# Optimization experiments

Measured on AMD Instinct MI355X. Metric: run time of the kernel, lower is better.

Reference implementation:

```python
import jax, jax.numpy as jnp
import numpy as np

B, N, DIM, HEADS, DH = 2, 1024, 1024, 16, 64
SEQ_LEN, MEM_NUM = 1024, 4
EH, EW, ET = 4, 4, 1  # mem_expand_size
PH, PW = 4, 4        # patch grid
CUR_PATCH_IDX = 5
MEM_IDXS = [0, 1, 4, 5]


def _locate(idx):
    # get_pos_from_idx_down_right
    num_frame = PH * PW
    inner = idx % num_frame
    return (inner % PH, inner // PH, idx // num_frame)


def _rel_idxs():
    rph, rpw = 2 * EH + 1, 2 * EW + 1
    frame = rph * rpw
    src = _locate(CUR_PATCH_IDX)
    out = []
    for t in MEM_IDXS + [CUR_PATCH_IDX]:
        tg = _locate(t)
        out.append((tg[0] - src[0] + EH) * rpw + (tg[1] - src[1] + EW) + (tg[2] - src[2] + ET) * frame)
    return np.array(out, np.int32)


def setup_inputs() -> dict:
    key = jax.random.key(0)
    ks = jax.random.split(key, 8)
    inner = HEADS * DH
    s = 0.02
    return {
        "x": jax.random.normal(ks[0], (B, N, DIM), jnp.float32),
        "mem": jax.random.normal(ks[1], (B, MEM_NUM * SEQ_LEN, DIM), jnp.float32),
        "mask": jnp.zeros((B, MEM_NUM * SEQ_LEN + N), bool),
        "rel_idxs": jnp.asarray(_rel_idxs()),
        "Wq": jax.random.normal(ks[2], (DIM, inner), jnp.float32) * s,
        "Wk": jax.random.normal(ks[3], (DIM, inner), jnp.float32) * s,
        "Wv": jax.random.normal(ks[4], (DIM, inner), jnp.float32) * s,
        "Wo": jax.random.normal(ks[5], (inner, DIM), jnp.float32) * s,
        "bo": jnp.zeros((DIM,), jnp.float32),
        "rel_table": jax.random.normal(ks[6], ((2 * EH + 1) * (2 * EW + 1) * (2 * ET + 1), HEADS), jnp.float32) * s,
    }


def reference(x, mem, mask, rel_idxs, Wq, Wk, Wv, Wo, bo, rel_table):
    b, n, dim = x.shape
    heads = rel_table.shape[1]
    dh = Wq.shape[1] // heads
    mem_num = rel_idxs.shape[0] - 1
    mem_len = mem.shape[1]
    seq_len = mem_len // mem_num
    scale = dh ** (-0.5)

    kx = jnp.concatenate([mem, x], axis=1)           # [b, j, dim]
    j = kx.shape[1]
    q = (x @ Wq).reshape(b, n, heads, dh).transpose(0, 2, 1, 3)   # bhid
    k = (kx @ Wk).reshape(b, j, heads, dh).transpose(0, 2, 1, 3)  # bhjd
    v = (kx @ Wv).reshape(b, j, heads, dh).transpose(0, 2, 1, 3)

    # relative position bias: a per-head scalar added to every K feature
    rel_emb = rel_table[rel_idxs].T                  # [h, mem_num+1]
    bias_mem = jnp.repeat(rel_emb[:, :mem_num], seq_len, axis=1)  # [h, mem_len]
    bias_cur = jnp.broadcast_to(rel_emb[:, -1:], (heads, j - mem_len))
    bias = jnp.concatenate([bias_mem, bias_cur], axis=1)          # [h, j]
    k = k + bias[None, :, :, None]

    dots = jnp.einsum('bhid,bhjd->bhij', q, k) * scale
    neg = -jnp.finfo(dots.dtype).max
    dots = jnp.where(mask[:, None, None, :], neg, dots)
    causal = jnp.triu(jnp.ones((n, j), bool), j - n + 1)
    dots = jnp.where(causal, neg, dots)

    attn = jax.nn.softmax(dots, axis=-1)
    out = jnp.einsum('bhij,bhjd->bhid', attn, v)
    out = out.transpose(0, 2, 1, 3).reshape(b, n, heads * dh) @ Wo + bo
    new_mem = x[:, -seq_len:]
    return out, new_mem
```

## Files before the change

kernel.cpp:

```cpp
#include <hip/hip_runtime.h>
#include <float.h>

#define NQ    1024
#define JTOT  5120
#define MEML  4096
#define SCL2  0.18033688011112042f

typedef __attribute__((ext_vector_type(8))) short bf16x8;
typedef __attribute__((ext_vector_type(8))) unsigned short ush8;
typedef __attribute__((ext_vector_type(4))) unsigned short ush4;
typedef __attribute__((ext_vector_type(4))) float f32x4;

static __device__ __forceinline__ unsigned short f2bf(float x) {
    union { float f; unsigned u; } v; v.f = x;
    unsigned r = (v.u + 0x7fffu + ((v.u >> 16) & 1u)) >> 16;
    return (unsigned short)r;
}
static __device__ __forceinline__ unsigned pack2(float f0, float f1) {
    union { float f; unsigned u; } a, b; a.f = f1; b.f = f0;
    return __builtin_amdgcn_perm(a.u, b.u, 0x07060302u);
}

static __device__ __forceinline__ void gld16(const void* g, void* l) {
    __builtin_amdgcn_global_load_lds(
        (const __attribute__((address_space(1))) unsigned int*)g,
        (__attribute__((address_space(3))) unsigned int*)l, 16, 0, 0);
}

__global__ __launch_bounds__(256)
void prep_kernel(const float* __restrict__ x, const float* __restrict__ mem,
                 const unsigned char* __restrict__ mask,
                 const float* __restrict__ W0, const float* __restrict__ W1,
                 const float* __restrict__ W2, const float* __restrict__ W3,
                 unsigned short* __restrict__ xb, unsigned short* __restrict__ memb,
                 unsigned short* __restrict__ wt, float* __restrict__ mbp)
{
    __shared__ float Ts[32][33];
    const int bid = blockIdx.x;
    const int t   = threadIdx.x;
    if (bid < 5120) {
        const float* src = (bid < 1024) ? x : mem;
        unsigned short* dst = (bid < 1024) ? xb : memb;
        const size_t i = (size_t)((bid < 1024) ? bid : bid - 1024) * 2048 + t * 8;
        float4 a = *(const float4*)(src + i);
        float4 b = *(const float4*)(src + i + 4);
        ush8 o;
        o[0] = f2bf(a.x); o[1] = f2bf(a.y); o[2] = f2bf(a.z); o[3] = f2bf(a.w);
        o[4] = f2bf(b.x); o[5] = f2bf(b.y); o[6] = f2bf(b.z); o[7] = f2bf(b.w);
        *(ush8*)(dst + i) = o;
    } else if (bid < 5160) {
        const int i = (bid - 5120) * 256 + t;
        mbp[i] = mask[i] ? -1.0e30f : 0.0f;
    } else {
        const int idx = bid - 5160;
        const int z   = idx >> 10;
        const int rem = idx & 1023;
        const float* W = (z == 0) ? W0 : (z == 1) ? W1 : (z == 2) ? W2 : W3;
        unsigned short* D = wt + (size_t)z * 1024 * 1024;
        const int n0 = (rem & 31) * 32, k0 = (rem >> 5) * 32;
        const int tr = t >> 3, tc = (t & 7) * 4;
        float4 v = *(const float4*)(W + (size_t)(k0 + tr) * 1024 + n0 + tc);
        Ts[tr][tc + 0] = v.x; Ts[tr][tc + 1] = v.y;
        Ts[tr][tc + 2] = v.z; Ts[tr][tc + 3] = v.w;
        __syncthreads();
        ush4 o;
        o[0] = f2bf(Ts[tc + 0][tr]); o[1] = f2bf(Ts[tc + 1][tr]);
        o[2] = f2bf(Ts[tc + 2][tr]); o[3] = f2bf(Ts[tc + 3][tr]);
        *(ush4*)(D + (size_t)(n0 + tr) * 1024 + k0 + tc) = o;
    }
}

__global__ __launch_bounds__(512, 2)
void mgemm01_kernel(const unsigned short* __restrict__ xb,
                    const unsigned short* __restrict__ memb,
                    const unsigned short* __restrict__ wt,
                    unsigned short* __restrict__ Qb, unsigned short* __restrict__ Kb,
                    unsigned short* __restrict__ Vb,
                    const float* __restrict__ rel_table, const int* __restrict__ rel_idxs)
{
    __shared__ unsigned short A1R0[128 * 64], A2R0[128 * 64];
    __shared__ unsigned short A1R1[128 * 64], A2R1[128 * 64];
    __shared__ unsigned short Bf0[256 * 64],  Bf1[256 * 64];

    const int t    = threadIdx.x;
    const int lane = t & 63;
    const int w    = t >> 6;
    const int wr   = w >> 2;
    const int wc   = w & 3;
    const int l15  = lane & 15;
    const int quad = lane >> 4;
    const int l7   = l15 & 7;
    const int srow = lane >> 3;
    const int scol = ((lane & 7) ^ srow) << 3;

    const int bid = blockIdx.x;
    int mode, bx, by;
    if (bid < 96) {
        mode = 0;
        const int l = (bid & 7) * 12 + (bid >> 3);
        bx = l >> 3;
        by = l & 7;
    } else {
        mode = 1;
        const int p   = bid - 96;
        const int xcd = p & 7;
        const int i   = p >> 3;
        bx = i & 7;
        by = (xcd << 2) + (i >> 3);
    }
    const int mat = bx >> 2;
    const int n0  = (bx & 3) << 8;
    const int m0  = by << 8;
    const unsigned short* Ag = (mode == 0) ? xb : memb;
    const unsigned short* Bg = wt + (size_t)((mode == 0) ? mat : mat + 1) * 1024 * 1024;

    const size_t abase = (size_t)(m0 + srow) * 1024 + scol;
    const size_t bbase = (size_t)(n0 + srow) * 1024 + scol;

    auto stgB0 = [&](unsigned short* BO, int kt) {
        const int kb = kt << 6, r0 = w * 16;
        gld16(Bg + bbase + (size_t)r0 * 1024 + kb,       BO + r0 * 64);
        gld16(Bg + bbase + (size_t)(r0 + 8) * 1024 + kb, BO + (r0 + 8) * 64);
    };
    auto stgB1 = [&](unsigned short* BO, int kt) {
        const int kb = kt << 6, r0 = 128 + w * 16;
        gld16(Bg + bbase + (size_t)r0 * 1024 + kb,       BO + r0 * 64);
        gld16(Bg + bbase + (size_t)(r0 + 8) * 1024 + kb, BO + (r0 + 8) * 64);
    };
    auto stgA1 = [&](unsigned short* AO, int kt) {
        const int kb = kt << 6, r0 = w * 8;
        gld16(Ag + abase + (size_t)r0 * 1024 + kb,         AO + r0 * 64);
        gld16(Ag + abase + (size_t)(128 + r0) * 1024 + kb, AO + (64 + r0) * 64);
    };
    auto stgA2 = [&](unsigned short* AO, int kt) {
        const int kb = kt << 6, r0 = w * 8;
        gld16(Ag + abase + (size_t)(64 + r0) * 1024 + kb,  AO + r0 * 64);
        gld16(Ag + abase + (size_t)(192 + r0) * 1024 + kb, AO + (64 + r0) * 64);
    };

    f32x4 acc[8][4];
    #pragma unroll
    for (int i = 0; i < 8; i++)
        #pragma unroll
        for (int j = 0; j < 4; j++) acc[i][j] = (f32x4){0.f, 0.f, 0.f, 0.f};

    stgB0(Bf0, 0); stgB1(Bf0, 0); stgA1(A1R0, 0); stgA2(A2R0, 0);
    stgB0(Bf1, 1); stgA1(A1R1, 1); stgB1(Bf1, 1);
    asm volatile("s_waitcnt vmcnt(6)");
    __builtin_amdgcn_s_barrier();

    bf16x8 bfr[4][2];

#define PHASE(AO, MB, STAGE, VMW)                                                  \
    {                                                                              \
        const int Ra0 = (wr * 64 + ((MB) & 3) * 16 + l15) * 64;                    \
        const int Ra1 = Ra0 + 16 * 64;                                             \
        const bf16x8 a0 = *(const bf16x8*)&AO[Ra0 + ((quad ^ l7) << 3)];           \
        const bf16x8 a1 = *(const bf16x8*)&AO[Ra0 + (((4 | quad) ^ l7) << 3)];     \
        const bf16x8 a2 = *(const bf16x8*)&AO[Ra1 + ((quad ^ l7) << 3)];           \
        const bf16x8 a3 = *(const bf16x8*)&AO[Ra1 + (((4 | quad) ^ l7) << 3)];     \
        STAGE;                                                                     \
        __builtin_amdgcn_s_barrier();                                              \
        asm volatile("s_waitcnt lgkmcnt(0)");                                      \
        __builtin_amdgcn_sched_barrier(0);                                         \
        __builtin_amdgcn_s_setprio(1);                                             \
        _Pragma("unroll")                                                          \
        for (int n = 0; n < 4; n++) {                                              \
            acc[(MB)][n]     = __builtin_amdgcn_mfma_f32_16x16x32_bf16(a0, bfr[n][0], acc[(MB)][n], 0, 0, 0);     \
            acc[(MB)][n]     = __builtin_amdgcn_mfma_f32_16x16x32_bf16(a1, bfr[n][1], acc[(MB)][n], 0, 0, 0);     \
            acc[(MB) + 1][n] = __builtin_amdgcn_mfma_f32_16x16x32_bf16(a2, bfr[n][0], acc[(MB) + 1][n], 0, 0, 0); \
            acc[(MB) + 1][n] = __builtin_amdgcn_mfma_f32_16x16x32_bf16(a3, bfr[n][1], acc[(MB) + 1][n], 0, 0, 0); \
        }                                                                          \
        __builtin_amdgcn_s_setprio(0);                                             \
        VMW;                                                                       \
        __builtin_amdgcn_s_barrier();                                              \
    }

#define KSTEP(A1O, A2O, BO, S0, S1, S2, S3, VMW)                                   \
    {                                                                              \
        _Pragma("unroll")                                                          \
        for (int n = 0; n < 4; n++) {                                              \
            const int Rb = (wc * 64 + n * 16 + l15) * 64;                          \
            bfr[n][0] = *(const bf16x8*)&BO[Rb + ((quad ^ l7) << 3)];              \
            bfr[n][1] = *(const bf16x8*)&BO[Rb + (((4 | quad) ^ l7) << 3)];        \
        }                                                                          \
        PHASE(A1O, 0, S0, (void)0)                                                 \
        PHASE(A1O, 2, S1, (void)0)                                                 \
        PHASE(A2O, 4, S2, (void)0)                                                 \
        PHASE(A2O, 6, S3, VMW)                                                     \
    }

    for (int e = 0; e < 14; e += 2) {
        KSTEP(A1R0, A2R0, Bf0,
              stgA2(A2R1, e + 1),
              stgB0(Bf0, e + 2),
              stgA1(A1R0, e + 2),
              stgB1(Bf0, e + 2),
              asm volatile("s_waitcnt vmcnt(6)"))
        KSTEP(A1R1, A2R1, Bf1,
              stgA2(A2R0, e + 2),
              stgB0(Bf1, e + 3),
              stgA1(A1R1, e + 3),
              stgB1(Bf1, e + 3),
              asm volatile("s_waitcnt vmcnt(6)"))
    }
    KSTEP(A1R0, A2R0, Bf0, stgA2(A2R1, 15), (void)0, (void)0, (void)0,
          asm volatile("s_waitcnt vmcnt(0)"))
    KSTEP(A1R1, A2R1, Bf1, (void)0, (void)0, (void)0, (void)0, (void)0)

#undef KSTEP
#undef PHASE

    const bool isQ = (mode == 0) && (mat == 0);
    const bool isK = (mode == 0) ? (mat == 1) : (mat == 0);
    if (!isQ && !isK) {
        #pragma unroll
        for (int m = 0; m < 8; m++) {
            const int r0 = m0 + wr * 128 + m * 16 + quad * 4;
            const int bb = (mode == 0) ? (r0 >> 10) : (r0 >> 12);
            const int j0 = (mode == 0) ? 4096 + (r0 & 1023) : (r0 & 4095);
            #pragma unroll
            for (int n = 0; n < 4; n++) {
                const int col = n0 + wc * 64 + n * 16 + l15;
                ush4 o;
                o[0] = f2bf(acc[m][n][0]); o[1] = f2bf(acc[m][n][1]);
                o[2] = f2bf(acc[m][n][2]); o[3] = f2bf(acc[m][n][3]);
                *(ush4*)(Vb + ((size_t)((bb * 16 + (col >> 6)) * 64 + (col & 63))) * JTOT + j0) = o;
            }
        }
    } else {
        #pragma unroll
        for (int m = 0; m < 8; m++)
            #pragma unroll
            for (int reg = 0; reg < 4; reg++) {
                const int r = m0 + wr * 128 + m * 16 + quad * 4 + reg;
                int bb, idx, chunk;
                if (mode == 0) { bb = r >> 10; idx = isK ? 4096 + (r & 1023) : (r & 1023); chunk = 4; }
                else           { bb = r >> 12; idx = r & 4095; chunk = idx >> 10; }
                #pragma unroll
                for (int n = 0; n < 4; n++) {
                    const int col = n0 + wc * 64 + n * 16 + l15;
                    const int hh = col >> 6, dh = col & 63;
                    float v = acc[m][n][reg];
                    if (isK) {
                        v += rel_table[rel_idxs[chunk] * 16 + hh];
                        Kb[((size_t)(bb * 16 + hh) * JTOT + idx) * 64 + dh] = f2bf(v);
                    } else {
                        Qb[((size_t)(bb * 16 + hh) * NQ + idx) * 64 + dh] = f2bf(v);
                    }
                }
            }
    }
}

__global__ __launch_bounds__(256)
void mgemm2_kernel(const unsigned short* __restrict__ A,
                   const unsigned short* __restrict__ WT,
                   float* __restrict__ outF, const float* __restrict__ bo,
                   const float* __restrict__ x, float* __restrict__ newmem)
{
    __shared__ unsigned short Al[64 * 64];
    __shared__ unsigned short Bl[128 * 64];

    const int t = threadIdx.x;
    if (blockIdx.z == 1) {
        const int blk = blockIdx.y * 8 + blockIdx.x;
        const size_t base = (size_t)blk * 8192 + t * 4;
        #pragma unroll
        for (int i = 0; i < 8; i++)
            *(float4*)(newmem + base + (size_t)i * 1024) =
                *(const float4*)(x + base + (size_t)i * 1024);
        return;
    }

    const int lane = t & 63;
    const int w    = t >> 6;
    const int l15  = lane & 15;
    const int quad = lane >> 4;
    const int l7   = l15 & 7;
    const int n0   = blockIdx.x * 128;
    const int m0   = blockIdx.y * 64;

    f32x4 acc[4][2];
    #pragma unroll
    for (int i = 0; i < 4; i++)
        #pragma unroll
        for (int j = 0; j < 2; j++) acc[i][j] = (f32x4){0.f, 0.f, 0.f, 0.f};

    for (int k0 = 0; k0 < 1024; k0 += 64) {
        __syncthreads();
        #pragma unroll
        for (int it = 0; it < 2; it++) {
            const int lin  = it * 256 + t;
            const int row  = lin >> 3;
            const int colb = ((lin & 7) ^ (row & 7)) * 8;
            gld16(A + (size_t)(m0 + row) * 1024 + k0 + colb,
                  &Al[(size_t)(it * 256 + w * 64) * 8]);
        }
        #pragma unroll
        for (int it = 0; it < 4; it++) {
            const int lin  = it * 256 + t;
            const int row  = lin >> 3;
            const int colb = ((lin & 7) ^ (row & 7)) * 8;
            gld16(WT + (size_t)(n0 + row) * 1024 + k0 + colb,
                  &Bl[(size_t)(it * 256 + w * 64) * 8]);
        }
        __syncthreads();
        bf16x8 af[4][2], bfr[2][2];
        #pragma unroll
        for (int i = 0; i < 4; i++) {
            const int R = i * 16 + l15;
            af[i][0] = *(const bf16x8*)&Al[R * 64 + ((quad ^ l7) << 3)];
            af[i][1] = *(const bf16x8*)&Al[R * 64 + (((4 | quad) ^ l7) << 3)];
        }
        #pragma unroll
        for (int j = 0; j < 2; j++) {
            const int R = w * 32 + j * 16 + l15;
            bfr[j][0] = *(const bf16x8*)&Bl[R * 64 + ((quad ^ l7) << 3)];
            bfr[j][1] = *(const bf16x8*)&Bl[R * 64 + (((4 | quad) ^ l7) << 3)];
        }
        #pragma unroll
        for (int i = 0; i < 4; i++)
            #pragma unroll
            for (int j = 0; j < 2; j++) {
                acc[i][j] = __builtin_amdgcn_mfma_f32_16x16x32_bf16(af[i][0], bfr[j][0], acc[i][j], 0, 0, 0);
                acc[i][j] = __builtin_amdgcn_mfma_f32_16x16x32_bf16(af[i][1], bfr[j][1], acc[i][j], 0, 0, 0);
            }
    }

    #pragma unroll
    for (int i = 0; i < 4; i++)
        #pragma unroll
        for (int reg = 0; reg < 4; reg++) {
            const int r = m0 + i * 16 + quad * 4 + reg;
            #pragma unroll
            for (int j = 0; j < 2; j++) {
                const int col = n0 + w * 32 + j * 16 + l15;
                outF[(size_t)r * 1024 + col] = acc[i][j][reg] + bo[col];
            }
        }
}

__global__ __launch_bounds__(256)
void attn5_kernel(const unsigned short* __restrict__ qh,
                  const unsigned short* __restrict__ kh,
                  const unsigned short* __restrict__ vt,
                  const float* __restrict__ mb,
                  unsigned short* __restrict__ ao)
{
    __shared__ unsigned short Ks[128 * 64];
    __shared__ unsigned short Vs[64 * 128];
    __shared__ unsigned short Ps[64 * 128];

    const int t    = threadIdx.x;
    const int lane = t & 63;
    const int w    = t >> 6;
    const int l15  = lane & 15;
    const int quad = lane >> 4;
    const int l7   = l15 & 7;
    const int qt   = blockIdx.x;
    const int h    = blockIdx.y;
    const int b    = blockIdx.z;
    const int qbase = qt * 64;
    const int qg    = qbase + w * 16 + l15;

    const unsigned short* qrow = qh + (((size_t)(b * 16 + h) * NQ + qg) << 6);
    const bf16x8 bq0 = *(const bf16x8*)(qrow + quad * 8);
    const bf16x8 bq1 = *(const bf16x8*)(qrow + 32 + quad * 8);

    const int krow = t >> 3;
    const int kcol = (t & 7) * 8;
    const int ksw  = ((t & 7) ^ (krow & 7)) * 8;
    const int vrow = t >> 4;
    const int vu   = t & 15;
    const int vcol = vu * 8;
    const int vsw  = ((vu & 8) | ((vu ^ (vrow & 7)) & 7)) * 8;

    const unsigned short* kbase = kh + (((size_t)(b * 16 + h) * JTOT) << 6);
    const unsigned short* vbase = vt + (((size_t)(b * 16 + h)) << 6) * JTOT;
    const float* mbb = mb + b * JTOT;

    f32x4 oa[4];
    #pragma unroll
    for (int mt = 0; mt < 4; mt++) oa[mt] = (f32x4){0.f, 0.f, 0.f, 0.f};
    float l_i = 0.f;

    const int ntp = (qt + 66) >> 1;

    ush8 kst[4], vst[4];
    #pragma unroll
    for (int p = 0; p < 4; p++)
        kst[p] = *(const ush8*)(kbase + ((size_t)(krow + 32 * p) << 6) + kcol);
    #pragma unroll
    for (int p = 0; p < 4; p++)
        vst[p] = *(const ush8*)(vbase + (size_t)(vrow + 16 * p) * JTOT + vcol);

    for (int jt = 0; jt < ntp; jt++) {
        const int jbase = jt * 128;
        __syncthreads();
        #pragma unroll
        for (int p = 0; p < 4; p++)
            *(ush8*)&Ks[(krow + 32 * p) * 64 + ksw] = kst[p];
        #pragma unroll
        for (int p = 0; p < 4; p++)
            *(ush8*)&Vs[(vrow + 16 * p) * 128 + vsw] = vst[p];
        __syncthreads();

        if (jt + 1 < ntp) {
            const int jb2 = jbase + 128;
            #pragma unroll
            for (int p = 0; p < 4; p++)
                kst[p] = *(const ush8*)(kbase + ((size_t)(jb2 + krow + 32 * p) << 6) + kcol);
            #pragma unroll
            for (int p = 0; p < 4; p++)
                vst[p] = *(const ush8*)(vbase + (size_t)(vrow + 16 * p) * JTOT + jb2 + vcol);
        }

        f32x4 sa[8];
        __builtin_amdgcn_s_setprio(1);
        #pragma unroll
        for (int mt2 = 0; mt2 < 8; mt2++) {
            const int ra = (mt2 * 16 + l15) * 64;
            const bf16x8 ak0 = *(const bf16x8*)&Ks[ra + ((quad ^ l7) << 3)];
            const bf16x8 ak1 = *(const bf16x8*)&Ks[ra + (((4 | quad) ^ l7) << 3)];
            f32x4 s = (f32x4){0.f, 0.f, 0.f, 0.f};
            s = __builtin_amdgcn_mfma_f32_16x16x32_bf16(ak0, bq0, s, 0, 0, 0);
            s = __builtin_amdgcn_mfma_f32_16x16x32_bf16(ak1, bq1, s, 0, 0, 0);
            sa[mt2] = s;
        }
        __builtin_amdgcn_s_setprio(0);

        #pragma unroll
        for (int mt2 = 0; mt2 < 8; mt2++) {
            const float4 mv = *(const float4*)(mbb + jbase + mt2 * 16 + quad * 4);
            sa[mt2][0] = sa[mt2][0] * SCL2 + mv.x;
            sa[mt2][1] = sa[mt2][1] * SCL2 + mv.y;
            sa[mt2][2] = sa[mt2][2] * SCL2 + mv.z;
            sa[mt2][3] = sa[mt2][3] * SCL2 + mv.w;
        }
        if (jt == ntp - 1) {
            const int tl = qg + 4096 - jbase;
            #pragma unroll
            for (int mt2 = 0; mt2 < 8; mt2++)
                #pragma unroll
                for (int r = 0; r < 4; r++)
                    if (mt2 * 16 + quad * 4 + r > tl) sa[mt2][r] = -1.0e30f;
        }

        #pragma unroll
        for (int mt2 = 0; mt2 < 8; mt2++)
            #pragma unroll
            for (int r = 0; r < 4; r++) {
                const float pv = __builtin_amdgcn_exp2f(sa[mt2][r]);
                sa[mt2][r] = pv;
                l_i += pv;
            }

        const int prow = (w * 16 + l15) * 128;
        #pragma unroll
        for (int mt2 = 0; mt2 < 8; mt2++) {
            const int u  = 2 * mt2 + (quad >> 1);
            const int up = (u & 8) | ((u ^ l7) & 7);
            uint2 pk;
            pk.x = pack2(sa[mt2][0], sa[mt2][1]);
            pk.y = pack2(sa[mt2][2], sa[mt2][3]);
            *(uint2*)&Ps[prow + up * 8 + (quad & 1) * 4] = pk;
        }

        __builtin_amdgcn_s_setprio(1);
        #pragma unroll
        for (int s = 0; s < 4; s++) {
            const int u  = quad + 4 * s;
            const int up = (u & 8) | ((u ^ l7) & 7);
            const bf16x8 bp = *(const bf16x8*)&Ps[prow + up * 8];
            #pragma unroll
            for (int mt = 0; mt < 4; mt++) {
                const bf16x8 av = *(const bf16x8*)&Vs[(mt * 16 + l15) * 128 + up * 8];
                oa[mt] = __builtin_amdgcn_mfma_f32_16x16x32_bf16(av, bp, oa[mt], 0, 0, 0);
            }
        }
        __builtin_amdgcn_s_setprio(0);
    }

    float l = l_i;
    l += __shfl_xor(l, 16);
    l += __shfl_xor(l, 32);
    const float inv = 1.0f / l;
    unsigned short* arow = ao + ((size_t)(b * NQ + qg)) * 1024 + h * 64;
    #pragma unroll
    for (int mt = 0; mt < 4; mt++) {
        ush4 o;
        o[0] = f2bf(oa[mt][0] * inv); o[1] = f2bf(oa[mt][1] * inv);
        o[2] = f2bf(oa[mt][2] * inv); o[3] = f2bf(oa[mt][3] * inv);
        *(ush4*)(arow + mt * 16 + quad * 4) = o;
    }
}

extern "C" void kernel_launch(void* const* d_in, const int* in_sizes, int n_in,
                              void* d_out, int out_size, void* d_ws, size_t ws_size,
                              hipStream_t stream)
{
    const float* x        = (const float*)d_in[0];
    const float* mem      = (const float*)d_in[1];
    const unsigned char* mask = (const unsigned char*)d_in[2];
    const int*   rel_idxs = (const int*)d_in[3];
    const float* Wq       = (const float*)d_in[4];
    const float* Wk       = (const float*)d_in[5];
    const float* Wv       = (const float*)d_in[6];
    const float* Wo       = (const float*)d_in[7];
    const float* bo       = (const float*)d_in[8];
    const float* rel_table= (const float*)d_in[9];

    float* out = (float*)d_out;
    const size_t M1 = (size_t)1024 * 1024;
    unsigned short* xb   = (unsigned short*)d_ws;
    unsigned short* memb = xb   + 2 * M1;
    unsigned short* wt   = memb + 8 * M1;
    unsigned short* qb   = wt   + 4 * M1;
    unsigned short* kb   = qb   + 2 * M1;
    unsigned short* vb   = kb   + 10 * M1;
    unsigned short* aob  = vb   + 10 * M1;
    float* mbp = (float*)(aob + 2 * M1);

    prep_kernel<<<9256, 256, 0, stream>>>(
        x, mem, mask, Wq, Wk, Wv, Wo, xb, memb, wt, mbp);
    mgemm01_kernel<<<352, 512, 0, stream>>>(
        xb, memb, wt, qb, kb, vb, rel_table, rel_idxs);
    attn5_kernel<<<dim3(16, 16, 2), 256, 0, stream>>>(qb, kb, vb, mbp, aob);
    mgemm2_kernel<<<dim3(8, 32, 2), 256, 0, stream>>>(
        aob, wt + 3 * M1, out, bo, x, out + (size_t)2048 * 1024);
}
```

Measured before the change: 304.0 us.

## Split QK^T across waves by key columns and remap blocks to XCDs

Each wave now computes scores for all 64 queries against its own 32-key slice of the K tile, rather than 16 queries against all 128 keys. This cuts redundant LDS reads of K and loads Q fragments for four query blocks per wave. An extra barrier is needed before the PV step, and row sums are reduced across waves through shared memory. Block indices are remapped so that head/batch pairs group by XCD, aiming for better L2 reuse of K/V.

Result: faster. 288.6 us (-5.1%).

```diff
diff --git a/kernel.cpp b/kernel.cpp
--- a/kernel.cpp
+++ b/kernel.cpp
@@ -342,7 +342,7 @@
 }
 
 __global__ __launch_bounds__(256)
-void attn5_kernel(const unsigned short* __restrict__ qh,
+void attn6_kernel(const unsigned short* __restrict__ qh,
                   const unsigned short* __restrict__ kh,
                   const unsigned short* __restrict__ vt,
                   const float* __restrict__ mb,
@@ -351,6 +351,7 @@
     __shared__ unsigned short Ks[128 * 64];
     __shared__ unsigned short Vs[64 * 128];
     __shared__ unsigned short Ps[64 * 128];
+    __shared__ float Ls[4][64];
 
     const int t    = threadIdx.x;
     const int lane = t & 63;
@@ -358,15 +359,26 @@
     const int l15  = lane & 15;
     const int quad = lane >> 4;
     const int l7   = l15 & 7;
-    const int qt   = blockIdx.x;
-    const int h    = blockIdx.y;
-    const int b    = blockIdx.z;
+
+    const int flat = blockIdx.x + 16 * blockIdx.y + 256 * blockIdx.z;
+    const int xcd  = flat & 7;
+    const int idx  = flat >> 3;
+    const int qt   = idx >> 2;
+    const int hb   = (xcd << 2) | (idx & 3);
+    const int h    = hb & 15;
+    const int b    = hb >> 4;
+
     const int qbase = qt * 64;
     const int qg    = qbase + w * 16 + l15;
 
-    const unsigned short* qrow = qh + (((size_t)(b * 16 + h) * NQ + qg) << 6);
-    const bf16x8 bq0 = *(const bf16x8*)(qrow + quad * 8);
-    const bf16x8 bq1 = *(const bf16x8*)(qrow + 32 + quad * 8);
+    bf16x8 bq0[4], bq1[4];
+    #pragma unroll
+    for (int qb = 0; qb < 4; qb++) {
+        const unsigned short* qrow =
+            qh + (((size_t)(b * 16 + h) * NQ + qbase + qb * 16 + l15) << 6);
+        bq0[qb] = *(const bf16x8*)(qrow + quad * 8);
+        bq1[qb] = *(const bf16x8*)(qrow + 32 + quad * 8);
+    }
 
     const int krow = t >> 3;
     const int kcol = (t & 7) * 8;
@@ -383,7 +395,7 @@
     f32x4 oa[4];
     #pragma unroll
     for (int mt = 0; mt < 4; mt++) oa[mt] = (f32x4){0.f, 0.f, 0.f, 0.f};
-    float l_i = 0.f;
+    float lacc[4] = {0.f, 0.f, 0.f, 0.f};
 
     const int ntp = (qt + 66) >> 1;
 
@@ -394,6 +406,8 @@
     #pragma unroll
     for (int p = 0; p < 4; p++)
         vst[p] = *(const ush8*)(vbase + (size_t)(vrow + 16 * p) * JTOT + vcol);
+
+    const int prow = (w * 16 + l15) * 128;
 
     for (int jt = 0; jt < ntp; jt++) {
         const int jbase = jt * 128;
@@ -416,56 +430,71 @@
                 vst[p] = *(const ush8*)(vbase + (size_t)(vrow + 16 * p) * JTOT + jb2 + vcol);
         }
 
-        f32x4 sa[8];
+        f32x4 sa[2][4];
         __builtin_amdgcn_s_setprio(1);
         #pragma unroll
-        for (int mt2 = 0; mt2 < 8; mt2++) {
-            const int ra = (mt2 * 16 + l15) * 64;
+        for (int kk = 0; kk < 2; kk++) {
+            const int mt2 = 2 * w + kk;
+            const int ra  = (mt2 * 16 + l15) * 64;
             const bf16x8 ak0 = *(const bf16x8*)&Ks[ra + ((quad ^ l7) << 3)];
             const bf16x8 ak1 = *(const bf16x8*)&Ks[ra + (((4 | quad) ^ l7) << 3)];
-            f32x4 s = (f32x4){0.f, 0.f, 0.f, 0.f};
-            s = __builtin_amdgcn_mfma_f32_16x16x32_bf16(ak0, bq0, s, 0, 0, 0);
-            s = __builtin_amdgcn_mfma_f32_16x16x32_bf16(ak1, bq1, s, 0, 0, 0);
-            sa[mt2] = s;
+            #pragma unroll
+            for (int qb = 0; qb < 4; qb++) {
+                f32x4 s = (f32x4){0.f, 0.f, 0.f, 0.f};
+                s = __builtin_amdgcn_mfma_f32_16x16x32_bf16(ak0, bq0[qb], s, 0, 0, 0);
+                s = __builtin_amdgcn_mfma_f32_16x16x32_bf16(ak1, bq1[qb], s, 0, 0, 0);
+                sa[kk][qb] = s;
+            }
         }
         __builtin_amdgcn_s_setprio(0);
 
         #pragma unroll
-        for (int mt2 = 0; mt2 < 8; mt2++) {
-            const float4 mv = *(const float4*)(mbb + jbase + mt2 * 16 + quad * 4);
-            sa[mt2][0] = sa[mt2][0] * SCL2 + mv.x;
-            sa[mt2][1] = sa[mt2][1] * SCL2 + mv.y;
-            sa[mt2][2] = sa[mt2][2] * SCL2 + mv.z;
-            sa[mt2][3] = sa[mt2][3] * SCL2 + mv.w;
+        for (int kk = 0; kk < 2; kk++) {
+            const float4 mv = *(const float4*)(mbb + jbase + (2 * w + kk) * 16 + quad * 4);
+            #pragma unroll
+            for (int qb = 0; qb < 4; qb++) {
+                sa[kk][qb][0] = sa[kk][qb][0] * SCL2 + mv.x;
+                sa[kk][qb][1] = sa[kk][qb][1] * SCL2 + mv.y;
+                sa[kk][qb][2] = sa[kk][qb][2] * SCL2 + mv.z;
+                sa[kk][qb][3] = sa[kk][qb][3] * SCL2 + mv.w;
+            }
         }
         if (jt == ntp - 1) {
-            const int tl = qg + 4096 - jbase;
-            #pragma unroll
-            for (int mt2 = 0; mt2 < 8; mt2++)
+            #pragma unroll
+            for (int qb = 0; qb < 4; qb++) {
+                const int tl = qbase + qb * 16 + l15 + 4096 - jbase;
                 #pragma unroll
-                for (int r = 0; r < 4; r++)
-                    if (mt2 * 16 + quad * 4 + r > tl) sa[mt2][r] = -1.0e30f;
-        }
-
-        #pragma unroll
-        for (int mt2 = 0; mt2 < 8; mt2++)
-            #pragma unroll
-            for (int r = 0; r < 4; r++) {
-                const float pv = __builtin_amdgcn_exp2f(sa[mt2][r]);
-                sa[mt2][r] = pv;
-                l_i += pv;
-            }
-
-        const int prow = (w * 16 + l15) * 128;
-        #pragma unroll
-        for (int mt2 = 0; mt2 < 8; mt2++) {
-            const int u  = 2 * mt2 + (quad >> 1);
+                for (int kk = 0; kk < 2; kk++)
+                    #pragma unroll
+                    for (int r = 0; r < 4; r++)
+                        if ((2 * w + kk) * 16 + quad * 4 + r > tl) sa[kk][qb][r] = -1.0e30f;
+            }
+        }
+
+        #pragma unroll
+        for (int kk = 0; kk < 2; kk++)
+            #pragma unroll
+            for (int qb = 0; qb < 4; qb++)
+                #pragma unroll
+                for (int r = 0; r < 4; r++) {
+                    const float pv = __builtin_amdgcn_exp2f(sa[kk][qb][r]);
+                    sa[kk][qb][r] = pv;
+                    lacc[qb] += pv;
+                }
+
+        #pragma unroll
+        for (int kk = 0; kk < 2; kk++) {
+            const int u  = 4 * w + 2 * kk + (quad >> 1);
             const int up = (u & 8) | ((u ^ l7) & 7);
-            uint2 pk;
-            pk.x = pack2(sa[mt2][0], sa[mt2][1]);
-            pk.y = pack2(sa[mt2][2], sa[mt2][3]);
-            *(uint2*)&Ps[prow + up * 8 + (quad & 1) * 4] = pk;
-        }
+            #pragma unroll
+            for (int qb = 0; qb < 4; qb++) {
+                uint2 pk;
+                pk.x = pack2(sa[kk][qb][0], sa[kk][qb][1]);
+                pk.y = pack2(sa[kk][qb][2], sa[kk][qb][3]);
+                *(uint2*)&Ps[(qb * 16 + l15) * 128 + up * 8 + (quad & 1) * 4] = pk;
+            }
+        }
+        __syncthreads();
 
         __builtin_amdgcn_s_setprio(1);
         #pragma unroll
@@ -482,9 +511,18 @@
         __builtin_amdgcn_s_setprio(0);
     }
 
-    float l = l_i;
-    l += __shfl_xor(l, 16);
-    l += __shfl_xor(l, 32);
+    #pragma unroll
+    for (int qb = 0; qb < 4; qb++) {
+        lacc[qb] += __shfl_xor(lacc[qb], 16);
+        lacc[qb] += __shfl_xor(lacc[qb], 32);
+    }
+    if (quad == 0) {
+        #pragma unroll
+        for (int qb = 0; qb < 4; qb++) Ls[w][qb * 16 + l15] = lacc[qb];
+    }
+    __syncthreads();
+    const float l = Ls[0][w * 16 + l15] + Ls[1][w * 16 + l15] +
+                    Ls[2][w * 16 + l15] + Ls[3][w * 16 + l15];
     const float inv = 1.0f / l;
     unsigned short* arow = ao + ((size_t)(b * NQ + qg)) * 1024 + h * 64;
     #pragma unroll
@@ -526,7 +564,7 @@
         x, mem, mask, Wq, Wk, Wv, Wo, xb, memb, wt, mbp);
     mgemm01_kernel<<<352, 512, 0, stream>>>(
         xb, memb, wt, qb, kb, vb, rel_table, rel_idxs);
-    attn5_kernel<<<dim3(16, 16, 2), 256, 0, stream>>>(qb, kb, vb, mbp, aob);
+    attn6_kernel<<<dim3(16, 16, 2), 256, 0, stream>>>(qb, kb, vb, mbp, aob);
     mgemm2_kernel<<<dim3(8, 32, 2), 256, 0, stream>>>(
         aob, wt + 3 * M1, out, bo, x, out + (size_t)2048 * 1024);
 }
```
